# Optimization experiments

Measured on AMD Instinct MI355X. Metric: run time of the kernel, lower is better.

## Reference

```python
import jax, jax.numpy as jnp
import numpy as np

N = 50000
E = 800000
D = 128


def setup_inputs() -> dict:
    key = jax.random.key(0)
    ks = jax.random.split(key, 10)
    x = jax.random.normal(ks[0], (N, D), dtype=jnp.float32)
    edge_index = jax.random.randint(ks[1], (2, E), 0, N, dtype=jnp.int32)
    s = 1.0 / np.sqrt(D)
    W1 = jax.random.uniform(ks[2], (D, D), jnp.float32, -s, s)
    b1 = jnp.zeros((D,), jnp.float32)
    W2 = jax.random.uniform(ks[3], (D, D), jnp.float32, -s, s)
    b2 = jnp.zeros((D,), jnp.float32)
    Wt = jax.random.uniform(ks[4], (D, 1), jnp.float32, -s, s)
    bt = jnp.zeros((1,), jnp.float32)
    We = jax.random.uniform(ks[5], (D, 1), jnp.float32, -s, s)
    be = jnp.zeros((1,), jnp.float32)
    return {"x": x, "edge_index": edge_index, "W1": W1, "b1": b1,
            "W2": W2, "b2": b2, "Wt": Wt, "bt": bt, "We": We, "be": be}


def _gcn_norm(edge_index, n):
    # add self-loops, then symmetric normalization D^-1/2 (A+I) D^-1/2
    loop = jnp.arange(n, dtype=edge_index.dtype)
    src = jnp.concatenate([edge_index[0], loop])
    dst = jnp.concatenate([edge_index[1], loop])
    ones = jnp.ones(src.shape[0], dtype=jnp.float32)
    deg = jax.ops.segment_sum(ones, dst, num_segments=n)
    dinv = jnp.where(deg > 0, jax.lax.rsqrt(deg), 0.0)
    norm = dinv[src] * dinv[dst]  # [E+N]
    return src, dst, norm


def _gcn_conv(h, W, b, src, dst, norm, n):
    h = h @ W                                   # [N, D'] dense GEMM
    msg = h[src] * norm[:, None]                # gather + scale
    out = jax.ops.segment_sum(msg, dst, num_segments=n)  # scatter-add
    return out + b


def reference(x, edge_index, W1, b1, W2, b2, Wt, bt, We, be):
    n = x.shape[0]
    src, dst, norm = _gcn_norm(edge_index, n)
    h = jax.nn.relu(_gcn_conv(x, W1, b1, src, dst, norm, n))
    h = jax.nn.relu(_gcn_conv(h, W2, b2, src, dst, norm, n))
    # dropout is identity at inference (eval mode)
    survival_time = h @ Wt + bt   # [N, 1]
    event_status = h @ We + be    # [N, 1]
    return survival_time, event_status
```

## Files before the change

### kernel.cpp

```cpp
#include <hip/hip_runtime.h>
#include <hip/hip_fp16.h>
#include <math.h>

#define NN 50000
#define NNP 50048
#define NE 800000
#define DD 128

#define NB  196
#define CAP 5300
#define CAPP 6400
#define EPB 4096
#define A_BLOCKS 196

#define SLAB2 (NNP * 64)

typedef _Float16 half8_t __attribute__((ext_vector_type(8)));
typedef float f32x4 __attribute__((ext_vector_type(4)));


__global__ __launch_bounds__(256) void k_setup(const int* __restrict__ src, const int* __restrict__ dst,
                                               int* __restrict__ bcnt, unsigned int* __restrict__ ebuf,
                                               const float* __restrict__ W1, const float* __restrict__ W2,
                                               __half* __restrict__ WT1, __half* __restrict__ WT2) {
    const int blk = blockIdx.x;
    const int tid = threadIdx.x;

    if (blk < A_BLOCKS) {
        __shared__ int hist[256];
        __shared__ int scanbuf[256];
        __shared__ int gbase[256];
        __shared__ unsigned int stage[EPB];
        __shared__ int tgt[EPB];

        const int e0 = blk * EPB;
        int nE = NE - e0; if (nE > EPB) nE = EPB;

        hist[tid] = 0;
        __syncthreads();

        unsigned int pk[16];
        unsigned int br[16];
        #pragma unroll
        for (int j = 0; j < 16; ++j) {
            int idx = tid + j * 256;
            if (idx < nE) {
                int e = e0 + idx;
                int s = src[e], d = dst[e];
                int b = d >> 8;
                int r = atomicAdd(&hist[b], 1);
                pk[j] = (unsigned int)s | ((unsigned int)(d & 255) << 16);
                br[j] = (unsigned int)b | ((unsigned int)r << 8);
            }
        }
        __syncthreads();
        int v = hist[tid];
        scanbuf[tid] = v;
        __syncthreads();
        for (int o = 1; o < 256; o <<= 1) {
            int t2 = (tid >= o) ? scanbuf[tid - o] : 0;
            __syncthreads();
            scanbuf[tid] += t2;
            __syncthreads();
        }
        int base_excl = scanbuf[tid] - v;
        if (tid < NB && v > 0) gbase[tid] = tid * CAP + atomicAdd(&bcnt[tid], v);
        hist[tid] = base_excl;
        __syncthreads();

        #pragma unroll
        for (int j = 0; j < 16; ++j) {
            int idx = tid + j * 256;
            if (idx < nE) {
                int b = br[j] & 255;
                int r = (int)(br[j] >> 8);
                int pos = hist[b] + r;
                stage[pos] = pk[j];
                tgt[pos]   = gbase[b] + r;
            }
        }
        __syncthreads();
        #pragma unroll
        for (int j = 0; j < 16; ++j) {
            int idx = tid + j * 256;
            if (idx < nE) ebuf[tgt[idx]] = stage[idx];
        }
    } else {
        const float* W  = (blk == A_BLOCKS) ? W1 : W2;
        __half*      WT = (blk == A_BLOCKS) ? WT1 : WT2;
        int n = tid >> 1;
        int k0 = (tid & 1) * 64;
        #pragma unroll 8
        for (int j = 0; j < 64; ++j) {
            int k = k0 + j;
            WT[n * DD + k] = __float2half(W[k * DD + n]);
        }
    }
}


__global__ __launch_bounds__(512) void k_build_csr(const unsigned int* __restrict__ ebuf,
                                                   const int* __restrict__ bcnt,
                                                   int* __restrict__ rowbeg, int* __restrict__ rowend,
                                                   float* __restrict__ dinv,
                                                   unsigned short* __restrict__ col) {
    __shared__ int cnt[256];
    __shared__ int scanb[256];
    __shared__ unsigned short stage[CAPP];

    const int b   = blockIdx.x;
    const int tid = threadIdx.x;
    const int seg0 = b * CAP;
    const int sb   = bcnt[b];
    const int n0   = b << 8;
    int nb = NN - n0; if (nb > 256) nb = 256;

    if (tid < 256) cnt[tid] = 0;
    __syncthreads();
    for (int p = tid; p < sb; p += 512) {
        unsigned int e = ebuf[seg0 + p];
        atomicAdd(&cnt[(e >> 16) & 255], 1);
    }
    __syncthreads();
    int v  = (tid < 256) ? cnt[tid] : 0;
    int pv = (v + 7) & ~7;
    if (tid < 256) scanb[tid] = pv;
    __syncthreads();
    for (int o = 1; o < 256; o <<= 1) {
        int t = 0;
        if (tid < 256 && tid >= o) t = scanb[tid - o];
        __syncthreads();
        if (tid < 256) scanb[tid] += t;
        __syncthreads();
    }
    int exclp = (tid < 256) ? (scanb[tid] - pv) : 0;
    if (tid < nb) {
        rowbeg[n0 + tid] = b * CAPP + exclp;
        rowend[n0 + tid] = b * CAPP + exclp + pv;
        dinv[n0 + tid] = rsqrtf(1.0f + (float)v);
    }
    if (tid < 256) cnt[tid] = exclp;
    __syncthreads();
    for (int p = tid; p < sb; p += 512) {
        unsigned int e = ebuf[seg0 + p];
        int pos = atomicAdd(&cnt[(e >> 16) & 255], 1);
        stage[pos] = (unsigned short)(e & 0xFFFFu);
    }
    __syncthreads();
    if (tid < nb) {
        for (int k = exclp + v; k < exclp + pv; ++k) stage[k] = (unsigned short)NN;
    }
    __syncthreads();
    const int sbp = scanb[255];
    for (int p = tid; p < sbp; p += 512) {
        col[b * CAPP + p] = stage[p];
    }
}


#define LPAD 136
#define GEMM_B 782
#define ZERO_B 98

__global__ __launch_bounds__(256) void k_gemm_x(const float* __restrict__ X, const __half* __restrict__ WT,
                                                const float* __restrict__ dinv, __half* __restrict__ Gc,
                                                float* __restrict__ zbuf, int zcount) {
    const int tid = threadIdx.x;

    if (blockIdx.x >= GEMM_B) {
        int idx = (blockIdx.x - GEMM_B) * 256 + tid;
        if (idx * 4 + 3 < zcount) ((float4*)zbuf)[idx] = make_float4(0.f, 0.f, 0.f, 0.f);
        else {
            for (int k = idx * 4; k < zcount; ++k) zbuf[k] = 0.f;
        }
        return;
    }

    __shared__ __half Wl[DD * LPAD];
    __shared__ __half Al[64 * LPAD];

    const int row0 = blockIdx.x * 64;

    {
        const uint4* WTg = (const uint4*)WT;
        #pragma unroll
        for (int j = 0; j < 8; ++j) {
            int u = tid + j * 256;
            int n = u >> 4, koff = (u & 15) * 8;
            uint4 v = WTg[u];
            *(uint4*)&Wl[n * LPAD + koff] = v;
        }
    }
    {
        const float4* X4 = (const float4*)X;
        #pragma unroll
        for (int j = 0; j < 8; ++j) {
            int u = tid + j * 256;
            int r = u >> 5, c4 = u & 31;
            int grow = row0 + r;
            float4 v = make_float4(0.f, 0.f, 0.f, 0.f);
            if (grow < NN) v = X4[(size_t)grow * 32 + c4];
            __half2 a = __floats2half2_rn(v.x, v.y);
            __half2 b = __floats2half2_rn(v.z, v.w);
            uint2 pk;
            pk.x = *(unsigned int*)&a;
            pk.y = *(unsigned int*)&b;
            *(uint2*)&Al[r * LPAD + c4 * 4] = pk;
        }
    }
    __syncthreads();

    const int wave = tid >> 6;
    const int lane = tid & 63;
    const int m    = lane & 15;
    const int quad = lane >> 4;

    f32x4 acc[8];
    #pragma unroll
    for (int t = 0; t < 8; ++t) acc[t] = (f32x4){0.f, 0.f, 0.f, 0.f};

    #pragma unroll
    for (int kk = 0; kk < DD; kk += 32) {
        half8_t a = *(const half8_t*)&Al[(wave * 16 + m) * LPAD + kk + quad * 8];
        #pragma unroll
        for (int t = 0; t < 8; ++t) {
            half8_t b = *(const half8_t*)&Wl[(t * 16 + m) * LPAD + kk + quad * 8];
            acc[t] = __builtin_amdgcn_mfma_f32_16x16x32_f16(a, b, acc[t], 0, 0, 0);
        }
    }

    __syncthreads();

    float4 dv = *(const float4*)&dinv[row0 + wave * 16 + quad * 4];

    #pragma unroll
    for (int t = 0; t < 8; ++t) {
        #pragma unroll
        for (int r = 0; r < 4; ++r) {
            int row_l = wave * 16 + quad * 4 + r;
            int c     = t * 16 + m;
            float val = acc[t][r] * ((const float*)&dv)[r];
            Al[row_l * LPAD + c] = __float2half(val);
        }
    }
    __syncthreads();

    {
        #pragma unroll
        for (int j = 0; j < 4; ++j) {
            int u = tid + j * 256;
            int r = u >> 4, c16 = u & 15;
            int ch = c16 >> 3, wi = c16 & 7;
            int grow = row0 + r;
            uint4 v = *(const uint4*)&Al[r * LPAD + c16 * 8];
            *(uint4*)(Gc + (size_t)ch * SLAB2 + (size_t)grow * 64 + wi * 8) = v;
        }
    }
}


__global__ __launch_bounds__(256) void k_gemm_h(const __half* __restrict__ Xc, const __half* __restrict__ WT,
                                                const float* __restrict__ dinv, __half* __restrict__ Gc) {
    __shared__ __half Wl[DD * LPAD];
    __shared__ __half Al[64 * LPAD];

    const int tid  = threadIdx.x;
    const int row0 = blockIdx.x * 64;

    {
        const uint4* WTg = (const uint4*)WT;
        #pragma unroll
        for (int j = 0; j < 8; ++j) {
            int u = tid + j * 256;
            int n = u >> 4, koff = (u & 15) * 8;
            uint4 v = WTg[u];
            *(uint4*)&Wl[n * LPAD + koff] = v;
        }
    }
    {
        #pragma unroll
        for (int j = 0; j < 4; ++j) {
            int u = tid + j * 256;
            int r = u >> 4, c16 = u & 15;
            int ch = c16 >> 3, wi = c16 & 7;
            int grow = row0 + r;
            uint4 v;
            if (grow < NN) v = *(const uint4*)(Xc + (size_t)ch * SLAB2 + (size_t)grow * 64 + wi * 8);
            else { v.x = 0; v.y = 0; v.z = 0; v.w = 0; }
            *(uint4*)&Al[r * LPAD + c16 * 8] = v;
        }
    }
    __syncthreads();

    const int wave = tid >> 6;
    const int lane = tid & 63;
    const int m    = lane & 15;
    const int quad = lane >> 4;

    f32x4 acc[8];
    #pragma unroll
    for (int t = 0; t < 8; ++t) acc[t] = (f32x4){0.f, 0.f, 0.f, 0.f};

    #pragma unroll
    for (int kk = 0; kk < DD; kk += 32) {
        half8_t a = *(const half8_t*)&Al[(wave * 16 + m) * LPAD + kk + quad * 8];
        #pragma unroll
        for (int t = 0; t < 8; ++t) {
            half8_t b = *(const half8_t*)&Wl[(t * 16 + m) * LPAD + kk + quad * 8];
            acc[t] = __builtin_amdgcn_mfma_f32_16x16x32_f16(a, b, acc[t], 0, 0, 0);
        }
    }

    __syncthreads();

    float4 dv = *(const float4*)&dinv[row0 + wave * 16 + quad * 4];

    #pragma unroll
    for (int t = 0; t < 8; ++t) {
        #pragma unroll
        for (int r = 0; r < 4; ++r) {
            int row_l = wave * 16 + quad * 4 + r;
            int c     = t * 16 + m;
            float val = acc[t][r] * ((const float*)&dv)[r];
            Al[row_l * LPAD + c] = __float2half(val);
        }
    }
    __syncthreads();

    {
        #pragma unroll
        for (int j = 0; j < 4; ++j) {
            int u = tid + j * 256;
            int r = u >> 4, c16 = u & 15;
            int ch = c16 >> 3, wi = c16 & 7;
            int grow = row0 + r;
            uint4 v = *(const uint4*)&Al[r * LPAD + c16 * 8];
            *(uint4*)(Gc + (size_t)ch * SLAB2 + (size_t)grow * 64 + wi * 8) = v;
        }
    }
}


__device__ inline float4 h4_to_f4(uint2 r) {
    __half2 a = *(__half2*)&r.x;
    __half2 b = *(__half2*)&r.y;
    float2 lo = __half22float2(a), hi = __half22float2(b);
    return make_float4(lo.x, lo.y, hi.x, hi.y);
}

__device__ inline uint2 f4_to_h4(float4 v) {
    __half2 a = __floats2half2_rn(v.x, v.y);
    __half2 b = __floats2half2_rn(v.z, v.w);
    uint2 r;
    r.x = *(unsigned int*)&a;
    r.y = *(unsigned int*)&b;
    return r;
}

__device__ inline float4 gather_grp64(const __half* __restrict__ slab, int node, int fl,
                                      const unsigned short* __restrict__ col, int beg, int end) {
    const __half* base = slab + fl * 4;
    float4 accA = h4_to_f4(*(const uint2*)(base + (size_t)node * 64));
    float4 accB = make_float4(0.f, 0.f, 0.f, 0.f);
    for (int p = beg; p < end; p += 8) {
        uint4 c8 = *(const uint4*)(col + p);
        int s0 = c8.x & 0xFFFF, s1 = c8.x >> 16;
        int s2 = c8.y & 0xFFFF, s3 = c8.y >> 16;
        int s4 = c8.z & 0xFFFF, s5 = c8.z >> 16;
        int s6 = c8.w & 0xFFFF, s7 = c8.w >> 16;
        float4 v0 = h4_to_f4(*(const uint2*)(base + (size_t)s0 * 64));
        float4 v1 = h4_to_f4(*(const uint2*)(base + (size_t)s1 * 64));
        float4 v2 = h4_to_f4(*(const uint2*)(base + (size_t)s2 * 64));
        float4 v3 = h4_to_f4(*(const uint2*)(base + (size_t)s3 * 64));
        float4 v4 = h4_to_f4(*(const uint2*)(base + (size_t)s4 * 64));
        float4 v5 = h4_to_f4(*(const uint2*)(base + (size_t)s5 * 64));
        float4 v6 = h4_to_f4(*(const uint2*)(base + (size_t)s6 * 64));
        float4 v7 = h4_to_f4(*(const uint2*)(base + (size_t)s7 * 64));
        accA.x += (v0.x + v1.x) + (v4.x + v5.x);
        accA.y += (v0.y + v1.y) + (v4.y + v5.y);
        accA.z += (v0.z + v1.z) + (v4.z + v5.z);
        accA.w += (v0.w + v1.w) + (v4.w + v5.w);
        accB.x += (v2.x + v3.x) + (v6.x + v7.x);
        accB.y += (v2.y + v3.y) + (v6.y + v7.y);
        accB.z += (v2.z + v3.z) + (v6.z + v7.z);
        accB.w += (v2.w + v3.w) + (v6.w + v7.w);
    }
    accA.x += accB.x; accA.y += accB.y; accA.z += accB.z; accA.w += accB.w;
    return accA;
}

__global__ __launch_bounds__(256) void k_aggregate_c(const __half* __restrict__ G, const float* __restrict__ dinv,
                                                     const int* __restrict__ rowbeg, const int* __restrict__ rowend,
                                                     const unsigned short* __restrict__ col,
                                                     const float* __restrict__ bias, __half* __restrict__ H) {
    const int bx    = blockIdx.x;
    const int slot  = bx & 7;
    const int chunk = slot >> 2;
    const int nb    = (bx >> 3) * 4 + (slot & 3);
    const int g     = threadIdx.x >> 4;
    const int fl    = threadIdx.x & 15;
    const int node  = nb * 16 + g;
    if (node >= NN) return;

    const __half* slab = G + (size_t)chunk * SLAB2;
    int beg = rowbeg[node];
    int end = rowend[node];
    float4 acc = gather_grp64(slab, node, fl, col, beg, end);

    float di = dinv[node];
    float4 bv = *(const float4*)(bias + chunk * 64 + fl * 4);
    float4 hv;
    hv.x = fmaxf(fmaf(di, acc.x, bv.x), 0.f);
    hv.y = fmaxf(fmaf(di, acc.y, bv.y), 0.f);
    hv.z = fmaxf(fmaf(di, acc.z, bv.z), 0.f);
    hv.w = fmaxf(fmaf(di, acc.w, bv.w), 0.f);
    *(uint2*)(H + (size_t)chunk * SLAB2 + (size_t)node * 64 + fl * 4) = f4_to_h4(hv);
}

__global__ __launch_bounds__(256) void k_aggregate_heads_c(const __half* __restrict__ G, const float* __restrict__ dinv,
                                                           const int* __restrict__ rowbeg, const int* __restrict__ rowend,
                                                           const unsigned short* __restrict__ col,
                                                           const float* __restrict__ bias,
                                                           const float* __restrict__ Wt, const float* __restrict__ bt,
                                                           const float* __restrict__ We, const float* __restrict__ be,
                                                           float* __restrict__ out) {
    const int bx    = blockIdx.x;
    const int slot  = bx & 7;
    const int chunk = slot >> 2;
    const int nb    = (bx >> 3) * 4 + (slot & 3);
    const int g     = threadIdx.x >> 4;
    const int fl    = threadIdx.x & 15;
    const int node  = nb * 16 + g;
    if (node >= NN) return;

    const __half* slab = G + (size_t)chunk * SLAB2;
    int beg = rowbeg[node];
    int end = rowend[node];
    float4 acc = gather_grp64(slab, node, fl, col, beg, end);

    float di = dinv[node];
    float4 bv = *(const float4*)(bias + chunk * 64 + fl * 4);
    float hx = fmaxf(fmaf(di, acc.x, bv.x), 0.f);
    float hy = fmaxf(fmaf(di, acc.y, bv.y), 0.f);
    float hz = fmaxf(fmaf(di, acc.z, bv.z), 0.f);
    float hw = fmaxf(fmaf(di, acc.w, bv.w), 0.f);

    float4 wt = *(const float4*)(Wt + chunk * 64 + fl * 4);
    float4 we = *(const float4*)(We + chunk * 64 + fl * 4);
    float t  = hx * wt.x + hy * wt.y + hz * wt.z + hw * wt.w;
    float ev = hx * we.x + hy * we.y + hz * we.z + hw * we.w;
    #pragma unroll
    for (int o = 1; o < 16; o <<= 1) {
        t  += __shfl_xor(t, o, 64);
        ev += __shfl_xor(ev, o, 64);
    }
    if (fl == 0) {
        if (chunk == 0) { t += bt[0]; ev += be[0]; }
        atomicAdd(&out[node], t);
        atomicAdd(&out[NN + node], ev);
    }
}


extern "C" void kernel_launch(void* const* d_in, const int* in_sizes, int n_in,
                              void* d_out, int out_size, void* d_ws, size_t ws_size,
                              hipStream_t stream) {
    const float* x  = (const float*)d_in[0];
    const int*   ei = (const int*)d_in[1];
    const float* W1 = (const float*)d_in[2];
    const float* b1 = (const float*)d_in[3];
    const float* W2 = (const float*)d_in[4];
    const float* b2 = (const float*)d_in[5];
    const float* Wt = (const float*)d_in[6];
    const float* bt = (const float*)d_in[7];
    const float* We = (const float*)d_in[8];
    const float* be = (const float*)d_in[9];
    float* out = (float*)d_out;

    const int* srcI = ei;
    const int* dstI = ei + NE;

    char* w = (char*)d_ws;
    __half*         Gh    = (__half*)w;         w += (size_t)2 * SLAB2 * sizeof(__half);
    __half*         H1h   = (__half*)w;         w += (size_t)2 * SLAB2 * sizeof(__half);
    __half*         WT1   = (__half*)w;         w += (size_t)DD * DD * sizeof(__half);
    __half*         WT2   = (__half*)w;         w += (size_t)DD * DD * sizeof(__half);
    unsigned int*   ebuf  = (unsigned int*)w;   w += (size_t)NB * CAP * sizeof(unsigned int);
    unsigned short* col   = (unsigned short*)w; w += (size_t)NB * CAPP * sizeof(unsigned short);
    float*          dinv  = (float*)w;          w += (size_t)(NN + 64) * sizeof(float);
    int*            rowbeg= (int*)w;            w += (size_t)NN * sizeof(int);
    int*            rowend= (int*)w;            w += (size_t)NN * sizeof(int);
    int*            bcnt  = (int*)w;            w += (size_t)NB * sizeof(int);

    const int SETUP_B = A_BLOCKS + 2;
    const int NBLK    = (NN + 15) / 16;
    const int AGG_B   = ((NBLK + 3) / 4) * 8;

    hipMemsetAsync(bcnt, 0, (size_t)NB * sizeof(int), stream);

    hipLaunchKernelGGL(k_setup,     dim3(SETUP_B), dim3(256), 0, stream,
                       srcI, dstI, bcnt, ebuf, W1, W2, WT1, WT2);
    hipLaunchKernelGGL(k_build_csr, dim3(NB),      dim3(512), 0, stream, ebuf, bcnt, rowbeg, rowend, dinv, col);

    hipLaunchKernelGGL(k_gemm_x,      dim3(GEMM_B + ZERO_B), dim3(256), 0, stream, x, WT1, dinv, Gh, out, out_size);
    hipLaunchKernelGGL(k_aggregate_c, dim3(AGG_B),           dim3(256), 0, stream, Gh, dinv, rowbeg, rowend, col, b1, H1h);

    hipLaunchKernelGGL(k_gemm_h,            dim3(GEMM_B), dim3(256), 0, stream, H1h, WT2, dinv, Gh);
    hipLaunchKernelGGL(k_aggregate_heads_c, dim3(AGG_B),  dim3(256), 0, stream, Gh, dinv, rowbeg, rowend, col, b2,
                       Wt, bt, We, be, out);
}
```

Measured before the change: 183.8 us.

## Replace global atomic bucket scatter with per-block run tables and fold dinv scaling

The setup kernel now writes each block's locally bucket-sorted edges contiguously, plus per-bucket counts and offsets, instead of using global atomics and scattered writes into fixed-capacity buckets. The CSR kernel scans the counts, gathers each bucket's runs from all setup blocks using a binary search over run starts, and stages them in shared memory. This removes the memset and global atomics at the cost of a larger shared-memory footprint and search overhead. Separately, the source-side dinv scaling moves from the second GEMM epilogue into the first aggregation's output, which is mathematically equivalent.

```diff
diff --git a/kernel.cpp b/kernel.cpp
--- a/kernel.cpp
+++ b/kernel.cpp
@@ -12,6 +12,7 @@
 #define CAPP 6400
 #define EPB 4096
 #define A_BLOCKS 196
+#define CSTRIDE 256
 
 #define SLAB2 (NNP * 64)
 
@@ -20,7 +21,8 @@
 
 
 __global__ __launch_bounds__(256) void k_setup(const int* __restrict__ src, const int* __restrict__ dst,
-                                               int* __restrict__ bcnt, unsigned int* __restrict__ ebuf,
+                                               unsigned int* __restrict__ ebuf2,
+                                               int* __restrict__ cnts, int* __restrict__ offs,
                                                const float* __restrict__ W1, const float* __restrict__ W2,
                                                __half* __restrict__ WT1, __half* __restrict__ WT2) {
     const int blk = blockIdx.x;
@@ -29,9 +31,7 @@
     if (blk < A_BLOCKS) {
         __shared__ int hist[256];
         __shared__ int scanbuf[256];
-        __shared__ int gbase[256];
         __shared__ unsigned int stage[EPB];
-        __shared__ int tgt[EPB];
 
         const int e0 = blk * EPB;
         int nE = NE - e0; if (nE > EPB) nE = EPB;
@@ -64,7 +64,10 @@
             __syncthreads();
         }
         int base_excl = scanbuf[tid] - v;
-        if (tid < NB && v > 0) gbase[tid] = tid * CAP + atomicAdd(&bcnt[tid], v);
+        if (tid < NB) {
+            cnts[blk * CSTRIDE + tid] = v;
+            offs[blk * CSTRIDE + tid] = base_excl;
+        }
         hist[tid] = base_excl;
         __syncthreads();
 
@@ -74,16 +77,14 @@
             if (idx < nE) {
                 int b = br[j] & 255;
                 int r = (int)(br[j] >> 8);
-                int pos = hist[b] + r;
-                stage[pos] = pk[j];
-                tgt[pos]   = gbase[b] + r;
+                stage[hist[b] + r] = pk[j];
             }
         }
         __syncthreads();
         #pragma unroll
         for (int j = 0; j < 16; ++j) {
             int idx = tid + j * 256;
-            if (idx < nE) ebuf[tgt[idx]] = stage[idx];
+            if (idx < nE) ebuf2[(size_t)blk * EPB + idx] = stage[idx];
         }
     } else {
         const float* W  = (blk == A_BLOCKS) ? W1 : W2;
@@ -99,27 +100,55 @@
 }
 
 
-__global__ __launch_bounds__(512) void k_build_csr(const unsigned int* __restrict__ ebuf,
-                                                   const int* __restrict__ bcnt,
-                                                   int* __restrict__ rowbeg, int* __restrict__ rowend,
-                                                   float* __restrict__ dinv,
-                                                   unsigned short* __restrict__ col) {
+__global__ __launch_bounds__(512) void k_csr(const unsigned int* __restrict__ ebuf2,
+                                             const int* __restrict__ cnts, const int* __restrict__ offs,
+                                             int* __restrict__ rowbeg, int* __restrict__ rowend,
+                                             float* __restrict__ dinv,
+                                             unsigned short* __restrict__ col) {
+    __shared__ int runp[256];
+    __shared__ int runoff[256];
     __shared__ int cnt[256];
     __shared__ int scanb[256];
-    __shared__ unsigned short stage[CAPP];
+    __shared__ unsigned int stage32[CAP];
+    __shared__ unsigned short colst[CAPP];
 
     const int b   = blockIdx.x;
     const int tid = threadIdx.x;
-    const int seg0 = b * CAP;
-    const int sb   = bcnt[b];
-    const int n0   = b << 8;
+    const int n0  = b << 8;
     int nb = NN - n0; if (nb > 256) nb = 256;
 
+    int len = 0;
+    if (tid < NB) {
+        len = cnts[tid * CSTRIDE + b];
+        runoff[tid] = offs[tid * CSTRIDE + b];
+    }
+    if (tid < 256) scanb[tid] = len;
+    __syncthreads();
+    for (int o = 1; o < 256; o <<= 1) {
+        int t = 0;
+        if (tid < 256 && tid >= o) t = scanb[tid - o];
+        __syncthreads();
+        if (tid < 256) scanb[tid] += t;
+        __syncthreads();
+    }
+    if (tid < 256) runp[tid] = scanb[tid] - len;
+    __syncthreads();
+    const int sb = scanb[255];
+
+    for (int p = tid; p < sb; p += 512) {
+        int lo = 0, hi = NB - 1;
+        while (lo < hi) {
+            int mid = (lo + hi + 1) >> 1;
+            if (runp[mid] <= p) lo = mid; else hi = mid - 1;
+        }
+        stage32[p] = ebuf2[(size_t)lo * EPB + runoff[lo] + (p - runp[lo])];
+    }
+    __syncthreads();
+
     if (tid < 256) cnt[tid] = 0;
     __syncthreads();
     for (int p = tid; p < sb; p += 512) {
-        unsigned int e = ebuf[seg0 + p];
-        atomicAdd(&cnt[(e >> 16) & 255], 1);
+        atomicAdd(&cnt[(stage32[p] >> 16) & 255], 1);
     }
     __syncthreads();
     int v  = (tid < 256) ? cnt[tid] : 0;
@@ -142,18 +171,18 @@
     if (tid < 256) cnt[tid] = exclp;
     __syncthreads();
     for (int p = tid; p < sb; p += 512) {
-        unsigned int e = ebuf[seg0 + p];
+        unsigned int e = stage32[p];
         int pos = atomicAdd(&cnt[(e >> 16) & 255], 1);
-        stage[pos] = (unsigned short)(e & 0xFFFFu);
+        colst[pos] = (unsigned short)(e & 0xFFFFu);
     }
     __syncthreads();
     if (tid < nb) {
-        for (int k = exclp + v; k < exclp + pv; ++k) stage[k] = (unsigned short)NN;
+        for (int k = exclp + v; k < exclp + pv; ++k) colst[k] = (unsigned short)NN;
     }
     __syncthreads();
     const int sbp = scanb[255];
     for (int p = tid; p < sbp; p += 512) {
-        col[b * CAPP + p] = stage[p];
+        col[b * CAPP + p] = colst[p];
     }
 }
 
@@ -260,7 +289,7 @@
 
 
 __global__ __launch_bounds__(256) void k_gemm_h(const __half* __restrict__ Xc, const __half* __restrict__ WT,
-                                                const float* __restrict__ dinv, __half* __restrict__ Gc) {
+                                                __half* __restrict__ Gc) {
     __shared__ __half Wl[DD * LPAD];
     __shared__ __half Al[64 * LPAD];
 
@@ -313,16 +342,13 @@
 
     __syncthreads();
 
-    float4 dv = *(const float4*)&dinv[row0 + wave * 16 + quad * 4];
-
     #pragma unroll
     for (int t = 0; t < 8; ++t) {
         #pragma unroll
         for (int r = 0; r < 4; ++r) {
             int row_l = wave * 16 + quad * 4 + r;
             int c     = t * 16 + m;
-            float val = acc[t][r] * ((const float*)&dv)[r];
-            Al[row_l * LPAD + c] = __float2half(val);
+            Al[row_l * LPAD + c] = __float2half(acc[t][r]);
         }
     }
     __syncthreads();
@@ -410,10 +436,10 @@
     float di = dinv[node];
     float4 bv = *(const float4*)(bias + chunk * 64 + fl * 4);
     float4 hv;
-    hv.x = fmaxf(fmaf(di, acc.x, bv.x), 0.f);
-    hv.y = fmaxf(fmaf(di, acc.y, bv.y), 0.f);
-    hv.z = fmaxf(fmaf(di, acc.z, bv.z), 0.f);
-    hv.w = fmaxf(fmaf(di, acc.w, bv.w), 0.f);
+    hv.x = di * fmaxf(fmaf(di, acc.x, bv.x), 0.f);
+    hv.y = di * fmaxf(fmaf(di, acc.y, bv.y), 0.f);
+    hv.z = di * fmaxf(fmaf(di, acc.z, bv.z), 0.f);
+    hv.w = di * fmaxf(fmaf(di, acc.w, bv.w), 0.f);
     *(uint2*)(H + (size_t)chunk * SLAB2 + (size_t)node * 64 + fl * 4) = f4_to_h4(hv);
 }
 
@@ -485,27 +511,27 @@
     __half*         H1h   = (__half*)w;         w += (size_t)2 * SLAB2 * sizeof(__half);
     __half*         WT1   = (__half*)w;         w += (size_t)DD * DD * sizeof(__half);
     __half*         WT2   = (__half*)w;         w += (size_t)DD * DD * sizeof(__half);
-    unsigned int*   ebuf  = (unsigned int*)w;   w += (size_t)NB * CAP * sizeof(unsigned int);
+    unsigned int*   ebuf2 = (unsigned int*)w;   w += (size_t)A_BLOCKS * EPB * sizeof(unsigned int);
     unsigned short* col   = (unsigned short*)w; w += (size_t)NB * CAPP * sizeof(unsigned short);
     float*          dinv  = (float*)w;          w += (size_t)(NN + 64) * sizeof(float);
     int*            rowbeg= (int*)w;            w += (size_t)NN * sizeof(int);
     int*            rowend= (int*)w;            w += (size_t)NN * sizeof(int);
-    int*            bcnt  = (int*)w;            w += (size_t)NB * sizeof(int);
+    int*            cnts  = (int*)w;            w += (size_t)A_BLOCKS * CSTRIDE * sizeof(int);
+    int*            offs  = (int*)w;            w += (size_t)A_BLOCKS * CSTRIDE * sizeof(int);
 
     const int SETUP_B = A_BLOCKS + 2;
     const int NBLK    = (NN + 15) / 16;
     const int AGG_B   = ((NBLK + 3) / 4) * 8;
 
-    hipMemsetAsync(bcnt, 0, (size_t)NB * sizeof(int), stream);
-
-    hipLaunchKernelGGL(k_setup,     dim3(SETUP_B), dim3(256), 0, stream,
-                       srcI, dstI, bcnt, ebuf, W1, W2, WT1, WT2);
-    hipLaunchKernelGGL(k_build_csr, dim3(NB),      dim3(512), 0, stream, ebuf, bcnt, rowbeg, rowend, dinv, col);
+    hipLaunchKernelGGL(k_setup, dim3(SETUP_B), dim3(256), 0, stream,
+                       srcI, dstI, ebuf2, cnts, offs, W1, W2, WT1, WT2);
+    hipLaunchKernelGGL(k_csr,   dim3(NB),      dim3(512), 0, stream,
+                       ebuf2, cnts, offs, rowbeg, rowend, dinv, col);
 
     hipLaunchKernelGGL(k_gemm_x,      dim3(GEMM_B + ZERO_B), dim3(256), 0, stream, x, WT1, dinv, Gh, out, out_size);
     hipLaunchKernelGGL(k_aggregate_c, dim3(AGG_B),           dim3(256), 0, stream, Gh, dinv, rowbeg, rowend, col, b1, H1h);
 
-    hipLaunchKernelGGL(k_gemm_h,            dim3(GEMM_B), dim3(256), 0, stream, H1h, WT2, dinv, Gh);
+    hipLaunchKernelGGL(k_gemm_h,            dim3(GEMM_B), dim3(256), 0, stream, H1h, WT2, Gh);
     hipLaunchKernelGGL(k_aggregate_heads_c, dim3(AGG_B),  dim3(256), 0, stream, Gh, dinv, rowbeg, rowend, col, b2,
                        Wt, bt, We, be, out);
 }
```

Result: no change. 186.9 us (+1.7%).
